# Optimization experiments

Measured on AMD Instinct MI355X. Metric: run time of the kernel, lower is better.

## Reference

```python
import jax, jax.numpy as jnp
import numpy as np

NH, HD, MB = 32, 64, 16        # heads, head_dim, TTT mini-batch size
BASE_LR = 1.0
ROPE_THETA = 10000.0


def _ln(x, w, b, eps):
    mu = x.mean(-1, keepdims=True)
    var = ((x - mu) ** 2).mean(-1, keepdims=True)
    return (x - mu) / jnp.sqrt(var + eps) * w + b


def _rotate_half(x):
    x1, x2 = jnp.split(x, 2, axis=-1)
    return jnp.concatenate([-x2, x1], axis=-1)


def _ln_l2_bwd(x, target, g, b, eps=1e-6):
    # grad of ||LN(x)*g+b - target||^2 / 2 wrt x (fused, as in ttt-lm)
    D = x.shape[-1]
    mu = x.mean(-1, keepdims=True)
    var = ((x - mu) ** 2).mean(-1, keepdims=True)
    std = jnp.sqrt(var + eps)
    xh = (x - mu) / std
    gxh = (g * xh + b - target) * g
    return (D * gxh - gxh.sum(-1, keepdims=True) - xh * (gxh * xh).sum(-1, keepdims=True)) / (D * std)


def _ttt_forward(x, q_w, k_w, v_w, o_w, ttt_lr_w, ttt_lr_b, token_idx_off,
                 ttt_norm_w, ttt_norm_b, W1, b1, post_w, post_b):
    B, L, C = x.shape
    NM = L // MB
    XQ = (x @ q_w).reshape(B, L, NH, HD).transpose(0, 2, 1, 3)  # [B,NH,L,HD]
    XK = (x @ k_w).reshape(B, L, NH, HD).transpose(0, 2, 1, 3)
    XV = (x @ v_w).reshape(B, L, NH, HD).transpose(0, 2, 1, 3)
    # rotary embedding at position_ids % mini_batch_size
    pos = (jnp.arange(L) % MB).astype(jnp.float32)
    inv = 1.0 / (ROPE_THETA ** (jnp.arange(0, HD, 2, dtype=jnp.float32) / HD))
    fr = pos[:, None] * inv[None, :]
    emb = jnp.concatenate([fr, fr], axis=-1)           # [L,HD]
    cos, sin = jnp.cos(emb), jnp.sin(emb)
    XQ = XQ * cos + _rotate_half(XQ) * sin
    XK = XK * cos + _rotate_half(XK) * sin
    # learning-rate gate (eta)
    Xm = x.reshape(B, NM, MB, C)
    ttt_lr = jax.nn.sigmoid(jnp.einsum('bnkc,hdc->bhnkd', Xm, ttt_lr_w)
                            + ttt_lr_b.reshape(1, NH, 1, 1, 1))       # [B,NH,NM,MB,1]
    ttt_lr_eta = BASE_LR * ttt_lr.transpose(0, 1, 2, 4, 3) / HD       # [B,NH,NM,1,MB]
    tok = jnp.maximum(1.0 / jnp.arange(1, MB + 1, dtype=jnp.float32) + token_idx_off, 0.0)
    eta = tok.reshape(1, 1, 1, MB, 1) * ttt_lr_eta                    # [B,NH,NM,MB,MB]

    def tomb(t):  # [B,NH,L,HD] -> [NM,B,NH,MB,HD]
        return t.reshape(B, NH, NM, MB, HD).transpose(2, 0, 1, 3, 4)

    xs = (tomb(XQ), tomb(XK), tomb(XV), eta.transpose(2, 0, 1, 3, 4))
    lw = ttt_norm_w.reshape(1, NH, 1, HD)
    lb = ttt_norm_b.reshape(1, NH, 1, HD)
    tril = jnp.tril(jnp.ones((MB, MB), x.dtype))
    W1s = jnp.broadcast_to(W1, (B, NH, HD, HD)).astype(x.dtype)
    b1s = jnp.broadcast_to(b1, (B, NH, 1, HD)).astype(x.dtype)

    def step(carry, xs_t):
        W1c, b1c = carry
        xq, xk, xv, et = xs_t                      # [B,NH,MB,HD], et [B,NH,MB,MB]
        Z1 = xk @ W1c + b1c
        grad = _ln_l2_bwd(Z1, xv - xk, lw, lb)     # grad of per-head TTT loss wrt Z1
        Attn1 = jnp.tril(xq @ xk.transpose(0, 1, 3, 2))
        b1_bar = b1c - (et * tril) @ grad
        Z1_bar = xq @ W1c - (et * Attn1) @ grad + b1_bar
        last_eta = et[:, :, -1, :, None]           # [B,NH,MB,1]
        W1n = W1c - jnp.einsum('bhki,bhkj->bhij', last_eta * xk, grad)
        b1n = b1c - (last_eta * grad).sum(-2, keepdims=True)
        out = xq + _ln(Z1_bar, lw, lb, 1e-6)
        return (W1n, b1n), out

    _, outs = jax.lax.scan(step, (W1s, b1s), xs)   # outs: [NM,B,NH,MB,HD]
    y = outs.transpose(1, 0, 3, 2, 4).reshape(B, L, C)
    y = _ln(y, post_w, post_b, 1e-6)
    return y @ o_w


def setup_inputs() -> dict:
    key = jax.random.key(0)
    ks = jax.random.split(key, 16)
    B, L, C, DH = 4, 2048, 2048, 1024
    s = 0.02
    return {
        'enc_input': jax.random.normal(ks[0], (B, L, C), jnp.float32),
        'ln1_w': jnp.ones((C,), jnp.float32), 'ln1_b': jnp.zeros((C,), jnp.float32),
        'q_w': jax.random.normal(ks[1], (C, C), jnp.float32) * s,
        'k_w': jax.random.normal(ks[2], (C, C), jnp.float32) * s,
        'v_w': jax.random.normal(ks[3], (C, C), jnp.float32) * s,
        'o_w': jax.random.normal(ks[4], (C, C), jnp.float32) * s,
        'ttt_lr_w': jax.random.normal(ks[5], (NH, 1, C), jnp.float32) * s,
        'ttt_lr_b': jax.random.normal(ks[6], (NH,), jnp.float32) * s,
        'token_idx_off': jax.random.normal(ks[7], (MB,), jnp.float32) * 0.01,
        'ttt_norm_w': jnp.ones((NH, HD), jnp.float32),
        'ttt_norm_b': jnp.zeros((NH, HD), jnp.float32),
        'W1': jax.random.normal(ks[8], (NH, HD, HD), jnp.float32) * s,
        'b1': jnp.zeros((NH, 1, HD), jnp.float32),
        'post_w': jnp.ones((C,), jnp.float32), 'post_b': jnp.zeros((C,), jnp.float32),
        'ffn_ln_w': jnp.ones((C,), jnp.float32), 'ffn_ln_b': jnp.zeros((C,), jnp.float32),
        'w1f': jax.random.normal(ks[9], (C, DH), jnp.float32) * s,
        'b1f': jnp.zeros((DH,), jnp.float32),
        'w2f': jax.random.normal(ks[10], (DH, C), jnp.float32) * s,
        'b2f': jnp.zeros((C,), jnp.float32),
    }


def reference(enc_input, ln1_w, ln1_b, q_w, k_w, v_w, o_w, ttt_lr_w, ttt_lr_b,
              token_idx_off, ttt_norm_w, ttt_norm_b, W1, b1, post_w, post_b,
              ffn_ln_w, ffn_ln_b, w1f, b1f, w2f, b2f):
    # pre-LN (torch default eps=1e-5) + TTT linear block + residual
    x = _ln(enc_input, ln1_w, ln1_b, 1e-5)
    y = _ttt_forward(x, q_w, k_w, v_w, o_w, ttt_lr_w, ttt_lr_b, token_idx_off,
                     ttt_norm_w, ttt_norm_b, W1, b1, post_w, post_b)
    y = y + enc_input
    # position-wise FFN (pre-LN eps=1e-6) + residual; dropout = eval no-op
    z = _ln(y, ffn_ln_w, ffn_ln_b, 1e-6)
    z = jax.nn.relu(z @ w1f + b1f) @ w2f + b2f
    return z + y
```

## Files before the change

kernel.cpp:

```cpp
#include <hip/hip_runtime.h>

typedef unsigned short u16;
typedef __attribute__((ext_vector_type(8))) short short8;
typedef __attribute__((ext_vector_type(8))) unsigned short ushort8;
typedef __attribute__((ext_vector_type(4))) float f32x4;
typedef __attribute__((ext_vector_type(2))) float f32x2;
typedef __attribute__((ext_vector_type(2))) unsigned int uint2v;

#define DEV __device__ __forceinline__

DEV float bf2f(u16 u){ union{unsigned int i; float f;} v; v.i = ((unsigned int)u)<<16u; return v.f; }
DEV u16 f2bf(float f){ union{float f; unsigned int i;} v; v.f=f; unsigned int r = v.i + 0x7FFFu + ((v.i>>16)&1u); return (u16)(r>>16); }

DEV void gload16(const u16* g, u16* l){
  __builtin_amdgcn_global_load_lds((const __attribute__((address_space(1))) void*)g,
                                   (__attribute__((address_space(3))) void*)l, 16, 0, 0);
}

DEV float wsum(float v){
  v += __shfl_xor(v, 32, 64);
  v += __shfl_xor(v, 16, 64);
  v += __shfl_xor(v, 8, 64);
  v += __shfl_xor(v, 4, 64);
  v += __shfl_xor(v, 2, 64);
  v += __shfl_xor(v, 1, 64);
  return v;
}

#if __has_builtin(__builtin_amdgcn_permlane16_swap) && __has_builtin(__builtin_amdgcn_permlane32_swap)
DEV float qsum(float v){
  unsigned u = __float_as_uint(v);
  uint2v a = __builtin_amdgcn_permlane16_swap(u, u, false, false);
  float s = __uint_as_float(a[0]) + __uint_as_float(a[1]);
  unsigned u2 = __float_as_uint(s);
  uint2v bsw = __builtin_amdgcn_permlane32_swap(u2, u2, false, false);
  return __uint_as_float(bsw[0]) + __uint_as_float(bsw[1]);
}
#else
DEV float qsum(float v){
  v += __shfl_xor(v, 16, 64);
  v += __shfl_xor(v, 32, 64);
  return v;
}
#endif

DEV float block_sum(float v, float* red){
  v = wsum(v);
  __syncthreads();
  if((threadIdx.x & 63u)==0) red[threadIdx.x>>6] = v;
  __syncthreads();
  return red[0]+red[1]+red[2]+red[3];
}

#define BARS() do{ asm volatile("s_waitcnt lgkmcnt(0)" ::: "memory"); \
  __builtin_amdgcn_s_barrier(); __builtin_amdgcn_sched_barrier(0); }while(0)

__global__ __launch_bounds__(256) void ln_row(
    const float* __restrict__ in, const float* __restrict__ w, const float* __restrict__ bb,
    float eps, u16* __restrict__ outb)
{
  __shared__ float red[4];
  const int row = blockIdx.x, t = threadIdx.x;
  const float* p = in + (size_t)row*2048 + t*8;
  f32x4 a = *(const f32x4*)p;
  f32x4 c = *(const f32x4*)(p+4);
  float s = a[0]+a[1]+a[2]+a[3]+c[0]+c[1]+c[2]+c[3];
  s = block_sum(s, red);
  float mu = s*(1.f/2048.f);
  float vs = 0.f;
  #pragma unroll
  for(int j=0;j<4;j++){ float d=a[j]-mu; vs += d*d; }
  #pragma unroll
  for(int j=0;j<4;j++){ float d=c[j]-mu; vs += d*d; }
  vs = block_sum(vs, red);
  float rstd = rsqrtf(vs*(1.f/2048.f) + eps);
  f32x4 w0 = *(const f32x4*)(w + t*8);
  f32x4 w1 = *(const f32x4*)(w + t*8 + 4);
  f32x4 b0 = *(const f32x4*)(bb + t*8);
  f32x4 b1 = *(const f32x4*)(bb + t*8 + 4);
  ushort8 o;
  #pragma unroll
  for(int j=0;j<4;j++) o[j]   = f2bf((a[j]-mu)*rstd*w0[j] + b0[j]);
  #pragma unroll
  for(int j=0;j<4;j++) o[j+4] = f2bf((c[j]-mu)*rstd*w1[j] + b1[j]);
  *(ushort8*)(outb + (size_t)row*2048 + t*8) = o;
}

__global__ __launch_bounds__(256) void transpose_cast(
    const float* __restrict__ src, u16* __restrict__ dst, int K, int N)
{
  __shared__ float tile[32][33];
  const int kb = blockIdx.x*32, nb = blockIdx.y*32;
  const int tx = threadIdx.x & 31, ty = threadIdx.x >> 5;
  #pragma unroll
  for(int i=0;i<4;i++){
    int k = ty + i*8;
    tile[k][tx] = src[(size_t)(kb+k)*N + nb + tx];
  }
  __syncthreads();
  #pragma unroll
  for(int i=0;i<4;i++){
    int nn = ty + i*8;
    dst[(size_t)(nb+nn)*K + kb + tx] = f2bf(tile[tx][nn]);
  }
}

__global__ __launch_bounds__(256) void cast_lrw(const float* __restrict__ lrw, u16* __restrict__ dst)
{
  int i = blockIdx.x*256 + threadIdx.x;
  if (i < 32*2048) dst[i] = f2bf(lrw[i]);
  else dst[i] = 0;
}

__global__ void rope_init(const float* __restrict__ tio, float* __restrict__ cosb,
                          float* __restrict__ sinb, float* __restrict__ tokb)
{
  int t = blockIdx.x*256 + threadIdx.x;
  if (t < 1024){
    int p = t>>6, d = t&63;
    float inv = powf(10000.f, -(float)(2*(d&31))/64.f);
    float fr = (float)p * inv;
    cosb[t] = cosf(fr);
    sinb[t] = sinf(fr);
  }
  if (blockIdx.x==0 && threadIdx.x<16)
    tokb[threadIdx.x] = fmaxf(1.f/(float)(threadIdx.x+1) + tio[threadIdx.x], 0.f);
}

#define MM(MI,NI,AA,BB) acc[MI][NI] = __builtin_amdgcn_mfma_f32_16x16x32_bf16(AA, BB, acc[MI][NI], 0, 0, 0)

#define RD_A(D,KH,MF) (*(const short8*)(ldsb + ((D)<<16) + ((KH)<<14) + (wm<<13) + ((MF)<<10) + loff))
#define RD_B(D,KH,NF) (*(const short8*)(ldsb + ((D)<<16) + 32768 + ((KH)<<14) + (wn<<12) + ((NF)<<10) + loff))

#define PHASE(D,KH,MH,RB,STG,VM) { \
  __builtin_amdgcn_sched_barrier(0); \
  if (RB){ b0 = RD_B(D,KH,0); b1 = RD_B(D,KH,1); b2 = RD_B(D,KH,2); b3 = RD_B(D,KH,3); } \
  short8 a0 = RD_A(D,KH,4*(MH)+0); \
  short8 a1 = RD_A(D,KH,4*(MH)+1); \
  short8 a2 = RD_A(D,KH,4*(MH)+2); \
  short8 a3 = RD_A(D,KH,4*(MH)+3); \
  STG; \
  __builtin_amdgcn_sched_barrier(0); \
  __builtin_amdgcn_s_barrier(); \
  asm volatile("s_waitcnt lgkmcnt(0)" ::: "memory"); \
  __builtin_amdgcn_sched_barrier(0); \
  __builtin_amdgcn_s_setprio(1); \
  MM(4*(MH)+0,0,a0,b0); MM(4*(MH)+1,0,a1,b0); MM(4*(MH)+2,0,a2,b0); MM(4*(MH)+3,0,a3,b0); \
  MM(4*(MH)+0,1,a0,b1); MM(4*(MH)+1,1,a1,b1); MM(4*(MH)+2,1,a2,b1); MM(4*(MH)+3,1,a3,b1); \
  MM(4*(MH)+0,2,a0,b2); MM(4*(MH)+1,2,a1,b2); MM(4*(MH)+2,2,a2,b2); MM(4*(MH)+3,2,a3,b2); \
  MM(4*(MH)+0,3,a0,b3); MM(4*(MH)+1,3,a1,b3); MM(4*(MH)+2,3,a2,b3); MM(4*(MH)+3,3,a3,b3); \
  __builtin_amdgcn_s_setprio(0); \
  if (VM){ asm volatile("s_waitcnt vmcnt(8)" ::: "memory"); } \
  __builtin_amdgcn_sched_barrier(0); \
  __builtin_amdgcn_s_barrier(); \
}

template<int EPI>
__global__ __launch_bounds__(512, 2) void gemm256(
    const u16* __restrict__ A, const u16* __restrict__ Bt,
    float* __restrict__ C, u16* __restrict__ Cb,
    const float* __restrict__ bias, const float* __restrict__ resid,
    int Nld, int Nreal, int K, int ntN)
{
  extern __shared__ u16 lds[];
  const int t = threadIdx.x, lane = t&63, wv = t>>6;
  const int wm = wv>>2, wn = wv&3;
  const int fr = lane&15, kq = lane>>4;

  int bid = blockIdx.x;
  {
    int nwg = gridDim.x;
    int q = nwg>>3, r = nwg&7;
    int x = bid&7, l = bid>>3;
    bid = (x<r) ? (x*(q+1)+l) : (r*(q+1)+(x-r)*q+l);
  }
  const int bm = bid/ntN, bn = bid%ntN;

  f32x4 acc[8][4];
  #pragma unroll
  for(int i=0;i<8;i++)
    #pragma unroll
    for(int j=0;j<4;j++) acc[i][j]=(f32x4){0.f,0.f,0.f,0.f};

  const u16* gA = A  + (size_t)(bm*256)*K;
  const u16* gB = Bt + (size_t)(bn*256)*K;

  const int Ls   = (t&7) ^ ((t>>3)&7);
  const int rstg = ((t>>3)<<1) | (Ls>>2);
  const int cstg = (Ls&3)<<3;
  u16* const ldsw = lds + (wv<<9);

  const int Plane = (((fr&1)<<2) | kq) ^ (fr>>1);
  const int loff  = ((fr>>1)<<7) | (Plane<<4);
  const char* const ldsb = (const char*)lds;

  auto stA = [&](int d, int kh, int kts){
    u16* lb = ldsw + (d<<15) + (kh<<13);
    const u16* g = gA + (size_t)rstg*K + kts + (kh<<5) + cstg;
    gload16(g, lb);
    gload16(g + ((size_t)K<<7), lb + 4096);
  };
  auto stB = [&](int d, int kh, int kts){
    u16* lb = ldsw + (d<<15) + 16384 + (kh<<13);
    const u16* g = gB + (size_t)rstg*K + kts + (kh<<5) + cstg;
    gload16(g, lb);
    gload16(g + ((size_t)K<<7), lb + 4096);
  };

  stA(0,0,0); stB(0,0,0); stA(0,1,0); stB(0,1,0); stA(1,0,64); stB(1,0,64);
  asm volatile("s_waitcnt vmcnt(8)" ::: "memory");
  __builtin_amdgcn_sched_barrier(0);
  __builtin_amdgcn_s_barrier();

  for (int kt = 0; kt < K; kt += 128){
    const int ktp = (kt+128 < K) ? kt+128 : 0;
    const int ktq = (kt+192 < K) ? kt+192 : kt+192-K;
    short8 b0={0},b1={0},b2={0},b3={0};
    PHASE(0,0,0,1, stA(1,1,kt+64), 0)
    PHASE(0,0,1,0, stB(1,1,kt+64), 1)
    PHASE(0,1,0,1, stA(0,0,ktp),   0)
    PHASE(0,1,1,0, stB(0,0,ktp),   1)
    PHASE(1,0,0,1, stA(0,1,ktp),   0)
    PHASE(1,0,1,0, stB(0,1,ktp),   1)
    PHASE(1,1,0,1, stA(1,0,ktq),   0)
    PHASE(1,1,1,0, stB(1,0,ktq),   1)
  }

  const int cr = (lane>>4)<<2, cc = lane&15;
  #pragma unroll
  for(int mi=0;mi<8;mi++){
    #pragma unroll
    for(int ni=0;ni<4;ni++){
      const int row0 = bm*256 + wm*128 + mi*16 + cr;
      const int col  = bn*256 + wn*64  + ni*16 + cc;
      if (col < Nreal){
        #pragma unroll
        for(int rr=0;rr<4;rr++){
          size_t idx = (size_t)(row0+rr)*Nld + col;
          float v = acc[mi][ni][rr];
          if (EPI==1 || EPI==3) v += resid[idx];
          if (EPI==2 || EPI==3) v += bias[col];
          if (EPI==2){ v = fmaxf(v, 0.f); Cb[idx] = f2bf(v); }
          else if (EPI==4){ Cb[idx] = f2bf(v); }
          else C[idx] = v;
        }
      }
    }
  }
}

#define W1LD 72
#define XLD  72
#define GTLD 40
#define EKLD 40
#define EALD 40
#define TLD  17

__global__ __launch_bounds__(512, 1) void ttt_scan(
    const u16* __restrict__ XQKV,
    const float* __restrict__ ropec, const float* __restrict__ ropes,
    const float* __restrict__ tokp,
    const float* __restrict__ nw, const float* __restrict__ nb,
    const float* __restrict__ lrb,
    const float* __restrict__ W1i,
    const float* __restrict__ b1i,
    float* __restrict__ Y)
{
  const int blk = blockIdx.x, b = blk>>5, h = blk&31;
  const int t = threadIdx.x, lane = t&63, wv = t>>6;
  const int fr = lane&15, quad = lane>>4;
  const int i0 = wv*2, i1 = i0+1;

  __shared__ u16 W1bf[2][64*W1LD];
  __shared__ u16 xqbf[2][16*XLD];
  __shared__ u16 xkbf[2][16*XLD];
  __shared__ u16 exkT[2][64*EKLD];
  __shared__ u16 gradTbf[64*GTLD];
  __shared__ u16 etaA[16*EALD];
  __shared__ float tgT[2][64*TLD];
  __shared__ float xqT[2][64*TLD];
  __shared__ float b1s[64];
  __shared__ f32x2 lwlb[64];
  __shared__ float lrs[2][16];
  __shared__ float tokl[16];

  const float lrbh = lrb[h];
  const float cc0 = ropec[i0*64 + lane], ss0 = ropes[i0*64 + lane];
  const float cc1 = ropec[i1*64 + lane], ss1 = ropes[i1*64 + lane];
  const float tok15 = tokp[15];
  const float ct = tok15*(1.f/64.f);
  const float sg = (lane<32)? -1.f : 1.f;

  f32x4 wf0, wf1, wf2, wf3;
  if (wv < 4){
    const float* wsrc = W1i + (size_t)h*4096;
    #pragma unroll
    for(int r=0;r<4;r++){
      int d = wv*16+quad*4+r;
      wf0[r] = wsrc[( 0+fr)*64 + d];
      wf1[r] = wsrc[(16+fr)*64 + d];
      wf2[r] = wsrc[(32+fr)*64 + d];
      wf3[r] = wsrc[(48+fr)*64 + d];
    }
    #pragma unroll
    for(int r=0;r<4;r++){
      int d = wv*16+quad*4+r;
      W1bf[0][d*W1LD +  0 + fr] = f2bf(wf0[r]);
      W1bf[0][d*W1LD + 16 + fr] = f2bf(wf1[r]);
      W1bf[0][d*W1LD + 32 + fr] = f2bf(wf2[r]);
      W1bf[0][d*W1LD + 48 + fr] = f2bf(wf3[r]);
    }
  }
  for(int i=t;i<64*24;i+=512){
    int rr=i/24, cp=16+i%24;
    gradTbf[rr*GTLD+cp]=0; exkT[0][rr*EKLD+cp]=0; exkT[1][rr*EKLD+cp]=0;
  }
  for(int i=t;i<16*24;i+=512){ int rr=i/24, cp=16+i%24; etaA[rr*EALD+cp]=0; }
  if (t<64){ b1s[t]=b1i[h*64+t]; lwlb[t]=(f32x2){nw[h*64+t], nb[h*64+t]}; }
  if (t<16) tokl[t]=tokp[t];

  auto stage = [&](int bf, u16 Pq0,u16 Pk0,u16 Pv0,u16 Pl0,
                           u16 Pq1,u16 Pk1,u16 Pv1,u16 Pl1){
    float q0=bf2f(Pq0), k0=bf2f(Pk0), v0=bf2f(Pv0);
    float q1=bf2f(Pq1), k1=bf2f(Pk1), v1=bf2f(Pv1);
    float qr0 = q0*cc0 + sg*__shfl_xor(q0,32,64)*ss0;
    float kr0 = k0*cc0 + sg*__shfl_xor(k0,32,64)*ss0;
    float qr1 = q1*cc1 + sg*__shfl_xor(q1,32,64)*ss1;
    float kr1 = k1*cc1 + sg*__shfl_xor(k1,32,64)*ss1;
    float lr0 = 1.f/(1.f + expf(-(bf2f(Pl0) + lrbh)));
    float lr1 = 1.f/(1.f + expf(-(bf2f(Pl1) + lrbh)));
    xqbf[bf][i0*XLD+lane] = f2bf(qr0);
    xqbf[bf][i1*XLD+lane] = f2bf(qr1);
    xkbf[bf][i0*XLD+lane] = f2bf(kr0);
    xkbf[bf][i1*XLD+lane] = f2bf(kr1);
    exkT[bf][lane*EKLD+i0] = f2bf(-ct*lr0*kr0);
    exkT[bf][lane*EKLD+i1] = f2bf(-ct*lr1*kr1);
    tgT[bf][lane*TLD+i0] = v0 - kr0;
    tgT[bf][lane*TLD+i1] = v1 - kr1;
    xqT[bf][lane*TLD+i0] = qr0;
    xqT[bf][lane*TLD+i1] = qr1;
    if (lane==0){ lrs[bf][i0]=lr0; lrs[bf][i1]=lr1; }
  };

  {
    const size_t rb = (size_t)b*2048;
    const u16* p0 = XQKV + (rb+i0)*6272 + h*64 + lane;
    const u16* p1 = XQKV + (rb+i1)*6272 + h*64 + lane;
    u16 l0 = XQKV[(rb+i0)*6272 + 6144 + h];
    u16 l1 = XQKV[(rb+i1)*6272 + 6144 + h];
    stage(0, p0[0],p0[2048],p0[4096],l0, p1[0],p1[2048],p1[4096],l1);
  }
  __syncthreads();

  const f32x4 fzero = (f32x4){0.f,0.f,0.f,0.f};

  for(int n=0;n<128;n++){
    const int cur = n&1, nxt = cur^1;
    const int cb = n&1, nbuf = cb^1;
    const size_t rbase = (size_t)b*2048 + n*16;

    u16 Pq0=0,Pk0=0,Pv0=0,Pl0=0,Pq1=0,Pk1=0,Pv1=0,Pl1=0;
    if (n<127){
      const size_t rb2 = rbase + 16;
      const u16* p0 = XQKV + (rb2+i0)*6272 + h*64 + lane;
      const u16* p1 = XQKV + (rb2+i1)*6272 + h*64 + lane;
      Pq0=p0[0]; Pk0=p0[2048]; Pv0=p0[4096];
      Pq1=p1[0]; Pk1=p1[2048]; Pv1=p1[4096];
      Pl0=XQKV[(rb2+i0)*6272 + 6144 + h];
      Pl1=XQKV[(rb2+i1)*6272 + 6144 + h];
    }

    f32x4 zq0, zq1, zq2, zq3;
    f32x4 b1q0, b1q1, b1q2, b1q3;
    float xq_r[16];
    f32x2 lw4[16];
    zq0=zq1=zq2=zq3=fzero; b1q0=b1q1=b1q2=b1q3=fzero;

    if (wv < 4){
      f32x4 b1v0 = *(const f32x4*)&b1s[ 0+quad*4];
      f32x4 b1v1 = *(const f32x4*)&b1s[16+quad*4];
      f32x4 b1v2 = *(const f32x4*)&b1s[32+quad*4];
      f32x4 b1v3 = *(const f32x4*)&b1s[48+quad*4];
      float tg[16]; f32x2 lwv[16];
      #pragma unroll
      for(int m=0;m<4;m++)
        #pragma unroll
        for(int r=0;r<4;r++){
          int d = m*16+quad*4+r;
          tg[m*4+r]  = tgT[cur][d*TLD + fr];
          lwv[m*4+r] = lwlb[d];
        }
      short8 bk0 = *(const short8*)&xkbf[cur][fr*XLD + quad*8];
      short8 bk1 = *(const short8*)&xkbf[cur][fr*XLD + 32 + quad*8];
      f32x4 z0,z1,z2,z3;
      z0 = __builtin_amdgcn_mfma_f32_16x16x32_bf16(*(const short8*)&W1bf[cb][( 0+fr)*W1LD + quad*8],      bk0, fzero, 0,0,0);
      z0 = __builtin_amdgcn_mfma_f32_16x16x32_bf16(*(const short8*)&W1bf[cb][( 0+fr)*W1LD + 32 + quad*8], bk1, z0,    0,0,0);
      z1 = __builtin_amdgcn_mfma_f32_16x16x32_bf16(*(const short8*)&W1bf[cb][(16+fr)*W1LD + quad*8],      bk0, fzero, 0,0,0);
      z1 = __builtin_amdgcn_mfma_f32_16x16x32_bf16(*(const short8*)&W1bf[cb][(16+fr)*W1LD + 32 + quad*8], bk1, z1,    0,0,0);
      z2 = __builtin_amdgcn_mfma_f32_16x16x32_bf16(*(const short8*)&W1bf[cb][(32+fr)*W1LD + quad*8],      bk0, fzero, 0,0,0);
      z2 = __builtin_amdgcn_mfma_f32_16x16x32_bf16(*(const short8*)&W1bf[cb][(32+fr)*W1LD + 32 + quad*8], bk1, z2,    0,0,0);
      z3 = __builtin_amdgcn_mfma_f32_16x16x32_bf16(*(const short8*)&W1bf[cb][(48+fr)*W1LD + quad*8],      bk0, fzero, 0,0,0);
      z3 = __builtin_amdgcn_mfma_f32_16x16x32_bf16(*(const short8*)&W1bf[cb][(48+fr)*W1LD + 32 + quad*8], bk1, z3,    0,0,0);
      f32x4 xh0,xh1,xh2,xh3;
      {
        float s1=0.f, s2=0.f;
        #pragma unroll
        for(int r=0;r<4;r++){
          z0[r] += b1v0[r];
          z1[r] += b1v1[r];
          z2[r] += b1v2[r];
          z3[r] += b1v3[r];
          s1 += z0[r]+z1[r]+z2[r]+z3[r];
          s2 += z0[r]*z0[r]+z1[r]*z1[r]+z2[r]*z2[r]+z3[r]*z3[r];
        }
        s1 = qsum(s1); s2 = qsum(s2);
        float mu = s1*(1.f/64.f);
        float var = s2*(1.f/64.f) - mu*mu;
        float rstd = rsqrtf(var + 1e-6f);
        float u1=0.f, u2=0.f;
        #pragma unroll
        for(int m=0;m<4;m++){
          f32x4* zp = (m==0)?&z0:(m==1)?&z1:(m==2)?&z2:&z3;
          f32x4* xp = (m==0)?&xh0:(m==1)?&xh1:(m==2)?&xh2:&xh3;
          #pragma unroll
          for(int r=0;r<4;r++){
            f32x2 wb = lwv[m*4+r];
            float xh = ((*zp)[r] - mu)*rstd;
            float gx = (wb[0]*xh + wb[1] - tg[m*4+r])*wb[0];
            (*xp)[r] = xh;
            (*zp)[r] = gx;
            u1 += gx; u2 += gx*xh;
          }
        }
        u1 = qsum(u1); u2 = qsum(u2);
        const float c64 = rstd*(1.f/64.f);
        #pragma unroll
        for(int m=0;m<4;m++){
          f32x4* zp = (m==0)?&z0:(m==1)?&z1:(m==2)?&z2:&z3;
          f32x4* xp = (m==0)?&xh0:(m==1)?&xh1:(m==2)?&xh2:&xh3;
          #pragma unroll
          for(int r=0;r<4;r++)
            (*zp)[r] = (64.f*(*zp)[r] - u1 - (*xp)[r]*u2)*c64;
        }
      }
      f32x4 zsel = (wv==0)?z0:(wv==1)?z1:(wv==2)?z2:z3;
      #pragma unroll
      for(int r=0;r<4;r++)
        gradTbf[(wv*16+quad*4+r)*GTLD + fr] = f2bf(zsel[r]);
      asm volatile("s_waitcnt lgkmcnt(0)" ::: "memory");
      short8 ga = *(const short8*)&gradTbf[(wv*16+fr)*GTLD + quad*8];
      short8 e0 = *(const short8*)&exkT[cur][( 0+fr)*EKLD + quad*8];
      short8 e1 = *(const short8*)&exkT[cur][(16+fr)*EKLD + quad*8];
      short8 e2 = *(const short8*)&exkT[cur][(32+fr)*EKLD + quad*8];
      short8 e3 = *(const short8*)&exkT[cur][(48+fr)*EKLD + quad*8];
      wf0 = __builtin_amdgcn_mfma_f32_16x16x32_bf16(ga, e0, wf0, 0,0,0);
      wf1 = __builtin_amdgcn_mfma_f32_16x16x32_bf16(ga, e1, wf1, 0,0,0);
      wf2 = __builtin_amdgcn_mfma_f32_16x16x32_bf16(ga, e2, wf2, 0,0,0);
      wf3 = __builtin_amdgcn_mfma_f32_16x16x32_bf16(ga, e3, wf3, 0,0,0);
      #pragma unroll
      for(int r=0;r<4;r++){
        int d = wv*16+quad*4+r;
        W1bf[nbuf][d*W1LD +  0 + fr] = f2bf(wf0[r]);
        W1bf[nbuf][d*W1LD + 16 + fr] = f2bf(wf1[r]);
        W1bf[nbuf][d*W1LD + 32 + fr] = f2bf(wf2[r]);
        W1bf[nbuf][d*W1LD + 48 + fr] = f2bf(wf3[r]);
      }
    }
    else if (wv == 4){
      b1q0 = *(const f32x4*)&b1s[ 0+quad*4];
      b1q1 = *(const f32x4*)&b1s[16+quad*4];
      b1q2 = *(const f32x4*)&b1s[32+quad*4];
      b1q3 = *(const f32x4*)&b1s[48+quad*4];
      #pragma unroll
      for(int m=0;m<4;m++)
        #pragma unroll
        for(int r=0;r<4;r++){
          int d = m*16+quad*4+r;
          xq_r[m*4+r] = xqT[cur][d*TLD + fr];
          lw4[m*4+r]  = lwlb[d];
        }
      short8 bq0 = *(const short8*)&xqbf[cur][fr*XLD + quad*8];
      short8 bq1 = *(const short8*)&xqbf[cur][fr*XLD + 32 + quad*8];
      zq0 = __builtin_amdgcn_mfma_f32_16x16x32_bf16(*(const short8*)&W1bf[cb][( 0+fr)*W1LD + quad*8],      bq0, fzero, 0,0,0);
      zq0 = __builtin_amdgcn_mfma_f32_16x16x32_bf16(*(const short8*)&W1bf[cb][( 0+fr)*W1LD + 32 + quad*8], bq1, zq0,   0,0,0);
      zq1 = __builtin_amdgcn_mfma_f32_16x16x32_bf16(*(const short8*)&W1bf[cb][(16+fr)*W1LD + quad*8],      bq0, fzero, 0,0,0);
      zq1 = __builtin_amdgcn_mfma_f32_16x16x32_bf16(*(const short8*)&W1bf[cb][(16+fr)*W1LD + 32 + quad*8], bq1, zq1,   0,0,0);
      zq2 = __builtin_amdgcn_mfma_f32_16x16x32_bf16(*(const short8*)&W1bf[cb][(32+fr)*W1LD + quad*8],      bq0, fzero, 0,0,0);
      zq2 = __builtin_amdgcn_mfma_f32_16x16x32_bf16(*(const short8*)&W1bf[cb][(32+fr)*W1LD + 32 + quad*8], bq1, zq2,   0,0,0);
      zq3 = __builtin_amdgcn_mfma_f32_16x16x32_bf16(*(const short8*)&W1bf[cb][(48+fr)*W1LD + quad*8],      bq0, fzero, 0,0,0);
      zq3 = __builtin_amdgcn_mfma_f32_16x16x32_bf16(*(const short8*)&W1bf[cb][(48+fr)*W1LD + 32 + quad*8], bq1, zq3,   0,0,0);
    }
    else if (wv == 7){
      short8 aq0 = *(const short8*)&xqbf[cur][fr*XLD + quad*8];
      short8 aq1 = *(const short8*)&xqbf[cur][fr*XLD + 32 + quad*8];
      short8 bk0 = *(const short8*)&xkbf[cur][fr*XLD + quad*8];
      short8 bk1 = *(const short8*)&xkbf[cur][fr*XLD + 32 + quad*8];
      f32x4 at;
      at = __builtin_amdgcn_mfma_f32_16x16x32_bf16(aq0, bk0, fzero, 0,0,0);
      at = __builtin_amdgcn_mfma_f32_16x16x32_bf16(aq1, bk1, at,    0,0,0);
      float lrj = lrs[cur][fr]*(1.f/64.f);
      #pragma unroll
      for(int r=0;r<4;r++){
        int i = quad*4 + r;
        float val = (fr <= i) ? -tokl[i]*lrj*(1.f + at[r]) : 0.f;
        etaA[i*EALD + fr] = f2bf(val);
      }
    }
    BARS();

    if (wv == 4){
      short8 be = *(const short8*)&etaA[fr*EALD + quad*8];
      f32x4 c20,c21,c22,c23;
      c20 = __builtin_amdgcn_mfma_f32_16x16x32_bf16(*(const short8*)&gradTbf[( 0+fr)*GTLD + quad*8], be, fzero, 0,0,0);
      c21 = __builtin_amdgcn_mfma_f32_16x16x32_bf16(*(const short8*)&gradTbf[(16+fr)*GTLD + quad*8], be, fzero, 0,0,0);
      c22 = __builtin_amdgcn_mfma_f32_16x16x32_bf16(*(const short8*)&gradTbf[(32+fr)*GTLD + quad*8], be, fzero, 0,0,0);
      c23 = __builtin_amdgcn_mfma_f32_16x16x32_bf16(*(const short8*)&gradTbf[(48+fr)*GTLD + quad*8], be, fzero, 0,0,0);
      f32x4 zb0,zb1,zb2,zb3;
      float s1=0.f, s2=0.f;
      #pragma unroll
      for(int r=0;r<4;r++){
        zb0[r] = zq0[r] + b1q0[r] + c20[r];
        zb1[r] = zq1[r] + b1q1[r] + c21[r];
        zb2[r] = zq2[r] + b1q2[r] + c22[r];
        zb3[r] = zq3[r] + b1q3[r] + c23[r];
        s1 += zb0[r]+zb1[r]+zb2[r]+zb3[r];
        s2 += zb0[r]*zb0[r]+zb1[r]*zb1[r]+zb2[r]*zb2[r]+zb3[r]*zb3[r];
      }
      s1 = qsum(s1); s2 = qsum(s2);
      float mu = s1*(1.f/64.f);
      float var = s2*(1.f/64.f) - mu*mu;
      float rstd = rsqrtf(var + 1e-6f);
      #pragma unroll
      for(int m=0;m<4;m++){
        f32x4* zp = (m==0)?&zb0:(m==1)?&zb1:(m==2)?&zb2:&zb3;
        f32x4 o;
        #pragma unroll
        for(int r=0;r<4;r++){
          f32x2 wb = lw4[m*4+r];
          float xh = ((*zp)[r] - mu)*rstd;
          o[r] = xq_r[m*4+r] + xh*wb[0] + wb[1];
        }
        *(f32x4*)&Y[(rbase+fr)*2048 + h*64 + m*16 + quad*4] = o;
      }
    }
    else if (wv == 5){
      const int d = lane;
      short8 g0 = *(const short8*)&gradTbf[d*GTLD + 0];
      short8 g1 = *(const short8*)&gradTbf[d*GTLD + 8];
      float s = 0.f;
      #pragma unroll
      for(int j=0;j<8;j++) s += lrs[cur][j]   * bf2f((u16)g0[j]);
      #pragma unroll
      for(int j=0;j<8;j++) s += lrs[cur][8+j] * bf2f((u16)g1[j]);
      b1s[d] -= ct * s;
    }
    if (n<127) stage(nxt, Pq0,Pk0,Pv0,Pl0, Pq1,Pk1,Pv1,Pl1);
    BARS();
  }
}

extern "C" void kernel_launch(void* const* d_in, const int* in_sizes, int n_in,
                              void* d_out, int out_size, void* d_ws, size_t ws_size,
                              hipStream_t stream)
{
  const float* enc   = (const float*)d_in[0];
  const float* ln1w  = (const float*)d_in[1];
  const float* ln1b  = (const float*)d_in[2];
  const float* qw    = (const float*)d_in[3];
  const float* kw    = (const float*)d_in[4];
  const float* vw    = (const float*)d_in[5];
  const float* ow    = (const float*)d_in[6];
  const float* lrw   = (const float*)d_in[7];
  const float* lrb   = (const float*)d_in[8];
  const float* tio   = (const float*)d_in[9];
  const float* tnw   = (const float*)d_in[10];
  const float* tnb   = (const float*)d_in[11];
  const float* W1i   = (const float*)d_in[12];
  const float* b1i   = (const float*)d_in[13];
  const float* postw = (const float*)d_in[14];
  const float* postb = (const float*)d_in[15];
  const float* flnw  = (const float*)d_in[16];
  const float* flnb  = (const float*)d_in[17];
  const float* w1f   = (const float*)d_in[18];
  const float* b1f   = (const float*)d_in[19];
  const float* w2f   = (const float*)d_in[20];
  const float* b2f   = (const float*)d_in[21];
  float* out = (float*)d_out;

  char* ws = (char*)d_ws;
  size_t off = 0;
  auto alloc = [&](size_t bytes)->void*{ void* p = ws + off; off += (bytes + 255) & ~(size_t)255; return p; };
  u16*   regA  = (u16*)  alloc(8192ull*2048*2);
  u16*   wqkvT = (u16*)  alloc(6400ull*2048*2);
  u16*   XQKV  = (u16*)  alloc(8192ull*6272*2);
  float* yb    = (float*)alloc(8192ull*2048*4);
  float* ropec = (float*)alloc(1024*4);
  float* ropes = (float*)alloc(1024*4);
  float* tokb  = (float*)alloc(64*4);

  u16* oT   = wqkvT;
  u16* w1fT = wqkvT + 2048ull*2048;
  u16* w2fT = w1fT + 1024ull*2048;
  u16* hbf  = XQKV;
  float* y2 = yb;

  static bool s_attr = false;
  if (!s_attr){
    s_attr = true;
    (void)hipFuncSetAttribute(reinterpret_cast<const void*>(gemm256<4>), hipFuncAttributeMaxDynamicSharedMemorySize, 131072);
    (void)hipFuncSetAttribute(reinterpret_cast<const void*>(gemm256<1>), hipFuncAttributeMaxDynamicSharedMemorySize, 131072);
    (void)hipFuncSetAttribute(reinterpret_cast<const void*>(gemm256<2>), hipFuncAttributeMaxDynamicSharedMemorySize, 131072);
    (void)hipFuncSetAttribute(reinterpret_cast<const void*>(gemm256<3>), hipFuncAttributeMaxDynamicSharedMemorySize, 131072);
  }

  rope_init<<<4, 256, 0, stream>>>(tio, ropec, ropes, tokb);

  dim3 tg1(64, 64);
  transpose_cast<<<tg1, 256, 0, stream>>>(qw, wqkvT,               2048, 2048);
  transpose_cast<<<tg1, 256, 0, stream>>>(kw, wqkvT + 2048ull*2048, 2048, 2048);
  transpose_cast<<<tg1, 256, 0, stream>>>(vw, wqkvT + 4096ull*2048, 2048, 2048);
  cast_lrw<<<2048, 256, 0, stream>>>(lrw, wqkvT + 6144ull*2048);

  ln_row<<<8192, 256, 0, stream>>>(enc, ln1w, ln1b, 1e-5f, regA);

  gemm256<4><<<32*25, 512, 131072, stream>>>(regA, wqkvT, nullptr, XQKV,
                                             nullptr, nullptr, 6272, 6272, 2048, 25);

  transpose_cast<<<tg1, 256, 0, stream>>>(ow, oT, 2048, 2048);
  dim3 tg2(64, 32);
  transpose_cast<<<tg2, 256, 0, stream>>>(w1f, w1fT, 2048, 1024);
  dim3 tg3(32, 64);
  transpose_cast<<<tg3, 256, 0, stream>>>(w2f, w2fT, 1024, 2048);

  ttt_scan<<<128, 512, 0, stream>>>(XQKV, ropec, ropes, tokb, tnw, tnb, lrb, W1i, b1i, yb);

  ln_row<<<8192, 256, 0, stream>>>(yb, postw, postb, 1e-6f, regA);
  gemm256<1><<<32*8, 512, 131072, stream>>>(regA, oT, y2, nullptr,
                                            nullptr, enc, 2048, 2048, 2048, 8);

  ln_row<<<8192, 256, 0, stream>>>(y2, flnw, flnb, 1e-6f, regA);
  gemm256<2><<<32*4, 512, 131072, stream>>>(regA, w1fT, nullptr, hbf,
                                            b1f, nullptr, 1024, 1024, 2048, 4);
  gemm256<3><<<32*8, 512, 131072, stream>>>(hbf, w2fT, out, nullptr,
                                            b2f, y2, 2048, 2048, 1024, 8);
}
```

Baseline: 857.1 us.

## Defer TTT output step by one mini-batch and split gradient across two waves

Restructures the per-mini-batch schedule in the TTT scan kernel. The output projection and norm for mini-batch n is deferred into iteration n+1, using double-buffered gradTbf and etaA, so it overlaps with the next gradient computation. The gradient/LN-backward work is also cut from four waves to two, with each producing two row blocks. Target and query tiles move to a row-major layout read with vector loads, and norm weights and token scales are kept in registers. This shortens the serial critical path per iteration at the cost of more shared memory and registers, and puts more work on fewer waves.

```diff
diff --git a/kernel.cpp b/kernel.cpp
--- a/kernel.cpp
+++ b/kernel.cpp
@@ -43,6 +43,8 @@
   return v;
 }
 #endif
+
+DEV float swap32(float v){ return __shfl_xor(v, 32, 64); }
 
 DEV float block_sum(float v, float* red){
   v = wsum(v);
@@ -254,7 +256,7 @@
 #define GTLD 40
 #define EKLD 40
 #define EALD 40
-#define TLD  17
+#define TD2  68
 
 __global__ __launch_bounds__(512, 1) void ttt_scan(
     const u16* __restrict__ XQKV,
@@ -275,21 +277,30 @@
   __shared__ u16 xqbf[2][16*XLD];
   __shared__ u16 xkbf[2][16*XLD];
   __shared__ u16 exkT[2][64*EKLD];
-  __shared__ u16 gradTbf[64*GTLD];
-  __shared__ u16 etaA[16*EALD];
-  __shared__ float tgT[2][64*TLD];
-  __shared__ float xqT[2][64*TLD];
+  __shared__ u16 gradTbf[2][64*GTLD];
+  __shared__ u16 etaA[2][16*EALD];
+  __shared__ float tgT2[2][16*TD2];
+  __shared__ float xqT2[2][16*TD2];
   __shared__ float b1s[64];
-  __shared__ f32x2 lwlb[64];
   __shared__ float lrs[2][16];
-  __shared__ float tokl[16];
 
   const float lrbh = lrb[h];
   const float cc0 = ropec[i0*64 + lane], ss0 = ropes[i0*64 + lane];
   const float cc1 = ropec[i1*64 + lane], ss1 = ropes[i1*64 + lane];
-  const float tok15 = tokp[15];
-  const float ct = tok15*(1.f/64.f);
+  const float ct = tokp[15]*(1.f/64.f);
   const float sg = (lane<32)? -1.f : 1.f;
+
+  f32x2 lwr[16];
+  #pragma unroll
+  for(int m=0;m<4;m++)
+    #pragma unroll
+    for(int r=0;r<4;r++){
+      int d = m*16+quad*4+r;
+      lwr[m*4+r] = (f32x2){nw[h*64+d], nb[h*64+d]};
+    }
+  float tki[4];
+  #pragma unroll
+  for(int r=0;r<4;r++) tki[r] = tokp[quad*4+r];
 
   f32x4 wf0, wf1, wf2, wf3;
   if (wv < 4){
@@ -313,20 +324,23 @@
   }
   for(int i=t;i<64*24;i+=512){
     int rr=i/24, cp=16+i%24;
-    gradTbf[rr*GTLD+cp]=0; exkT[0][rr*EKLD+cp]=0; exkT[1][rr*EKLD+cp]=0;
-  }
-  for(int i=t;i<16*24;i+=512){ int rr=i/24, cp=16+i%24; etaA[rr*EALD+cp]=0; }
-  if (t<64){ b1s[t]=b1i[h*64+t]; lwlb[t]=(f32x2){nw[h*64+t], nb[h*64+t]}; }
-  if (t<16) tokl[t]=tokp[t];
+    gradTbf[0][rr*GTLD+cp]=0; gradTbf[1][rr*GTLD+cp]=0;
+    exkT[0][rr*EKLD+cp]=0;    exkT[1][rr*EKLD+cp]=0;
+  }
+  for(int i=t;i<16*24;i+=512){
+    int rr=i/24, cp=16+i%24;
+    etaA[0][rr*EALD+cp]=0; etaA[1][rr*EALD+cp]=0;
+  }
+  if (t<64) b1s[t]=b1i[h*64+t];
 
   auto stage = [&](int bf, u16 Pq0,u16 Pk0,u16 Pv0,u16 Pl0,
                            u16 Pq1,u16 Pk1,u16 Pv1,u16 Pl1){
     float q0=bf2f(Pq0), k0=bf2f(Pk0), v0=bf2f(Pv0);
     float q1=bf2f(Pq1), k1=bf2f(Pk1), v1=bf2f(Pv1);
-    float qr0 = q0*cc0 + sg*__shfl_xor(q0,32,64)*ss0;
-    float kr0 = k0*cc0 + sg*__shfl_xor(k0,32,64)*ss0;
-    float qr1 = q1*cc1 + sg*__shfl_xor(q1,32,64)*ss1;
-    float kr1 = k1*cc1 + sg*__shfl_xor(k1,32,64)*ss1;
+    float qr0 = q0*cc0 + sg*swap32(q0)*ss0;
+    float kr0 = k0*cc0 + sg*swap32(k0)*ss0;
+    float qr1 = q1*cc1 + sg*swap32(q1)*ss1;
+    float kr1 = k1*cc1 + sg*swap32(k1)*ss1;
     float lr0 = 1.f/(1.f + expf(-(bf2f(Pl0) + lrbh)));
     float lr1 = 1.f/(1.f + expf(-(bf2f(Pl1) + lrbh)));
     xqbf[bf][i0*XLD+lane] = f2bf(qr0);
@@ -335,10 +349,10 @@
     xkbf[bf][i1*XLD+lane] = f2bf(kr1);
     exkT[bf][lane*EKLD+i0] = f2bf(-ct*lr0*kr0);
     exkT[bf][lane*EKLD+i1] = f2bf(-ct*lr1*kr1);
-    tgT[bf][lane*TLD+i0] = v0 - kr0;
-    tgT[bf][lane*TLD+i1] = v1 - kr1;
-    xqT[bf][lane*TLD+i0] = qr0;
-    xqT[bf][lane*TLD+i1] = qr1;
+    tgT2[bf][i0*TD2+lane] = v0 - kr0;
+    tgT2[bf][i1*TD2+lane] = v1 - kr1;
+    xqT2[bf][i0*TD2+lane] = qr0;
+    xqT2[bf][i1*TD2+lane] = qr1;
     if (lane==0){ lrs[bf][i0]=lr0; lrs[bf][i1]=lr1; }
   };
 
@@ -354,9 +368,53 @@
 
   const f32x4 fzero = (f32x4){0.f,0.f,0.f,0.f};
 
+  f32x4 zqP0=fzero, zqP1=fzero, zqP2=fzero, zqP3=fzero;
+  f32x4 b1qP0=fzero, b1qP1=fzero, b1qP2=fzero, b1qP3=fzero;
+
+  auto do_out = [&](int pbuf, size_t rb){
+    short8 be = *(const short8*)&etaA[pbuf][fr*EALD + quad*8];
+    f32x4 c20,c21,c22,c23;
+    c20 = __builtin_amdgcn_mfma_f32_16x16x32_bf16(*(const short8*)&gradTbf[pbuf][( 0+fr)*GTLD + quad*8], be, fzero, 0,0,0);
+    c21 = __builtin_amdgcn_mfma_f32_16x16x32_bf16(*(const short8*)&gradTbf[pbuf][(16+fr)*GTLD + quad*8], be, fzero, 0,0,0);
+    c22 = __builtin_amdgcn_mfma_f32_16x16x32_bf16(*(const short8*)&gradTbf[pbuf][(32+fr)*GTLD + quad*8], be, fzero, 0,0,0);
+    c23 = __builtin_amdgcn_mfma_f32_16x16x32_bf16(*(const short8*)&gradTbf[pbuf][(48+fr)*GTLD + quad*8], be, fzero, 0,0,0);
+    f32x4 xqv0 = *(const f32x4*)&xqT2[pbuf][fr*TD2 +  0 + quad*4];
+    f32x4 xqv1 = *(const f32x4*)&xqT2[pbuf][fr*TD2 + 16 + quad*4];
+    f32x4 xqv2 = *(const f32x4*)&xqT2[pbuf][fr*TD2 + 32 + quad*4];
+    f32x4 xqv3 = *(const f32x4*)&xqT2[pbuf][fr*TD2 + 48 + quad*4];
+    f32x4 zb0,zb1,zb2,zb3;
+    float s1=0.f, s2=0.f;
+    #pragma unroll
+    for(int r=0;r<4;r++){
+      zb0[r] = zqP0[r] + b1qP0[r] + c20[r];
+      zb1[r] = zqP1[r] + b1qP1[r] + c21[r];
+      zb2[r] = zqP2[r] + b1qP2[r] + c22[r];
+      zb3[r] = zqP3[r] + b1qP3[r] + c23[r];
+      s1 += zb0[r]+zb1[r]+zb2[r]+zb3[r];
+      s2 += zb0[r]*zb0[r]+zb1[r]*zb1[r]+zb2[r]*zb2[r]+zb3[r]*zb3[r];
+    }
+    s1 = qsum(s1); s2 = qsum(s2);
+    float mu = s1*(1.f/64.f);
+    float var = s2*(1.f/64.f) - mu*mu;
+    float rstd = rsqrtf(var + 1e-6f);
+    #pragma unroll
+    for(int m=0;m<4;m++){
+      f32x4* zp = (m==0)?&zb0:(m==1)?&zb1:(m==2)?&zb2:&zb3;
+      const f32x4* xp = (m==0)?&xqv0:(m==1)?&xqv1:(m==2)?&xqv2:&xqv3;
+      f32x4 o;
+      #pragma unroll
+      for(int r=0;r<4;r++){
+        f32x2 wb = lwr[m*4+r];
+        float xh = ((*zp)[r] - mu)*rstd;
+        o[r] = (*xp)[r] + xh*wb[0] + wb[1];
+      }
+      *(f32x4*)&Y[(rb+fr)*2048 + h*64 + m*16 + quad*4] = o;
+    }
+  };
+
   for(int n=0;n<128;n++){
-    const int cur = n&1, nxt = cur^1;
-    const int cb = n&1, nbuf = cb^1;
+    const int cur = n&1, nxt = cur^1, pb = cur^1;
+    const int cb = cur, nbuf = cur^1;
     const size_t rbase = (size_t)b*2048 + n*16;
 
     u16 Pq0=0,Pk0=0,Pv0=0,Pl0=0,Pq1=0,Pk1=0,Pv1=0,Pl1=0;
@@ -370,26 +428,15 @@
       Pl1=XQKV[(rb2+i1)*6272 + 6144 + h];
     }
 
-    f32x4 zq0, zq1, zq2, zq3;
-    f32x4 b1q0, b1q1, b1q2, b1q3;
-    float xq_r[16];
-    f32x2 lw4[16];
-    zq0=zq1=zq2=zq3=fzero; b1q0=b1q1=b1q2=b1q3=fzero;
-
-    if (wv < 4){
+    if (wv < 2){
       f32x4 b1v0 = *(const f32x4*)&b1s[ 0+quad*4];
       f32x4 b1v1 = *(const f32x4*)&b1s[16+quad*4];
       f32x4 b1v2 = *(const f32x4*)&b1s[32+quad*4];
       f32x4 b1v3 = *(const f32x4*)&b1s[48+quad*4];
-      float tg[16]; f32x2 lwv[16];
-      #pragma unroll
-      for(int m=0;m<4;m++)
-        #pragma unroll
-        for(int r=0;r<4;r++){
-          int d = m*16+quad*4+r;
-          tg[m*4+r]  = tgT[cur][d*TLD + fr];
-          lwv[m*4+r] = lwlb[d];
-        }
+      f32x4 tgv0 = *(const f32x4*)&tgT2[cur][fr*TD2 +  0 + quad*4];
+      f32x4 tgv1 = *(const f32x4*)&tgT2[cur][fr*TD2 + 16 + quad*4];
+      f32x4 tgv2 = *(const f32x4*)&tgT2[cur][fr*TD2 + 32 + quad*4];
+      f32x4 tgv3 = *(const f32x4*)&tgT2[cur][fr*TD2 + 48 + quad*4];
       short8 bk0 = *(const short8*)&xkbf[cur][fr*XLD + quad*8];
       short8 bk1 = *(const short8*)&xkbf[cur][fr*XLD + 32 + quad*8];
       f32x4 z0,z1,z2,z3;
@@ -422,11 +469,12 @@
         for(int m=0;m<4;m++){
           f32x4* zp = (m==0)?&z0:(m==1)?&z1:(m==2)?&z2:&z3;
           f32x4* xp = (m==0)?&xh0:(m==1)?&xh1:(m==2)?&xh2:&xh3;
+          const f32x4* tp = (m==0)?&tgv0:(m==1)?&tgv1:(m==2)?&tgv2:&tgv3;
           #pragma unroll
           for(int r=0;r<4;r++){
-            f32x2 wb = lwv[m*4+r];
+            f32x2 wb = lwr[m*4+r];
             float xh = ((*zp)[r] - mu)*rstd;
-            float gx = (wb[0]*xh + wb[1] - tg[m*4+r])*wb[0];
+            float gx = (wb[0]*xh + wb[1] - (*tp)[r])*wb[0];
             (*xp)[r] = xh;
             (*zp)[r] = gx;
             u1 += gx; u2 += gx*xh;
@@ -443,12 +491,54 @@
             (*zp)[r] = (64.f*(*zp)[r] - u1 - (*xp)[r]*u2)*c64;
         }
       }
-      f32x4 zsel = (wv==0)?z0:(wv==1)?z1:(wv==2)?z2:z3;
+      f32x4 zA = (wv==0)? z0 : z2;
+      f32x4 zB = (wv==0)? z1 : z3;
+      const int rb0 = wv*32;
       #pragma unroll
-      for(int r=0;r<4;r++)
-        gradTbf[(wv*16+quad*4+r)*GTLD + fr] = f2bf(zsel[r]);
-      asm volatile("s_waitcnt lgkmcnt(0)" ::: "memory");
-      short8 ga = *(const short8*)&gradTbf[(wv*16+fr)*GTLD + quad*8];
+      for(int r=0;r<4;r++){
+        gradTbf[cur][(rb0+quad*4+r)*GTLD + fr]    = f2bf(zA[r]);
+        gradTbf[cur][(rb0+16+quad*4+r)*GTLD + fr] = f2bf(zB[r]);
+      }
+    }
+    else if (wv == 4){
+      short8 bq0 = *(const short8*)&xqbf[cur][fr*XLD + quad*8];
+      short8 bq1 = *(const short8*)&xqbf[cur][fr*XLD + 32 + quad*8];
+      f32x4 zqN0,zqN1,zqN2,zqN3;
+      zqN0 = __builtin_amdgcn_mfma_f32_16x16x32_bf16(*(const short8*)&W1bf[cb][( 0+fr)*W1LD + quad*8],      bq0, fzero, 0,0,0);
+      zqN0 = __builtin_amdgcn_mfma_f32_16x16x32_bf16(*(const short8*)&W1bf[cb][( 0+fr)*W1LD + 32 + quad*8], bq1, zqN0,  0,0,0);
+      zqN1 = __builtin_amdgcn_mfma_f32_16x16x32_bf16(*(const short8*)&W1bf[cb][(16+fr)*W1LD + quad*8],      bq0, fzero, 0,0,0);
+      zqN1 = __builtin_amdgcn_mfma_f32_16x16x32_bf16(*(const short8*)&W1bf[cb][(16+fr)*W1LD + 32 + quad*8], bq1, zqN1,  0,0,0);
+      zqN2 = __builtin_amdgcn_mfma_f32_16x16x32_bf16(*(const short8*)&W1bf[cb][(32+fr)*W1LD + quad*8],      bq0, fzero, 0,0,0);
+      zqN2 = __builtin_amdgcn_mfma_f32_16x16x32_bf16(*(const short8*)&W1bf[cb][(32+fr)*W1LD + 32 + quad*8], bq1, zqN2,  0,0,0);
+      zqN3 = __builtin_amdgcn_mfma_f32_16x16x32_bf16(*(const short8*)&W1bf[cb][(48+fr)*W1LD + quad*8],      bq0, fzero, 0,0,0);
+      zqN3 = __builtin_amdgcn_mfma_f32_16x16x32_bf16(*(const short8*)&W1bf[cb][(48+fr)*W1LD + 32 + quad*8], bq1, zqN3,  0,0,0);
+      if (n > 0) do_out(pb, rbase - 16);
+      zqP0=zqN0; zqP1=zqN1; zqP2=zqN2; zqP3=zqN3;
+      b1qP0 = *(const f32x4*)&b1s[ 0+quad*4];
+      b1qP1 = *(const f32x4*)&b1s[16+quad*4];
+      b1qP2 = *(const f32x4*)&b1s[32+quad*4];
+      b1qP3 = *(const f32x4*)&b1s[48+quad*4];
+    }
+    else if (wv == 7){
+      short8 aq0 = *(const short8*)&xqbf[cur][fr*XLD + quad*8];
+      short8 aq1 = *(const short8*)&xqbf[cur][fr*XLD + 32 + quad*8];
+      short8 bk0 = *(const short8*)&xkbf[cur][fr*XLD + quad*8];
+      short8 bk1 = *(const short8*)&xkbf[cur][fr*XLD + 32 + quad*8];
+      f32x4 at;
+      at = __builtin_amdgcn_mfma_f32_16x16x32_bf16(aq0, bk0, fzero, 0,0,0);
+      at = __builtin_amdgcn_mfma_f32_16x16x32_bf16(aq1, bk1, at,    0,0,0);
+      float lrj = lrs[cur][fr]*(1.f/64.f);
+      #pragma unroll
+      for(int r=0;r<4;r++){
+        int i = quad*4 + r;
+        float val = (fr <= i) ? -tki[r]*lrj*(1.f + at[r]) : 0.f;
+        etaA[cur][i*EALD + fr] = f2bf(val);
+      }
+    }
+    BARS();
+
+    if (wv < 4){
+      short8 ga = *(const short8*)&gradTbf[cur][(wv*16+fr)*GTLD + quad*8];
       short8 e0 = *(const short8*)&exkT[cur][( 0+fr)*EKLD + quad*8];
       short8 e1 = *(const short8*)&exkT[cur][(16+fr)*EKLD + quad*8];
       short8 e2 = *(const short8*)&exkT[cur][(32+fr)*EKLD + quad*8];
@@ -466,87 +556,10 @@
         W1bf[nbuf][d*W1LD + 48 + fr] = f2bf(wf3[r]);
       }
     }
-    else if (wv == 4){
-      b1q0 = *(const f32x4*)&b1s[ 0+quad*4];
-      b1q1 = *(const f32x4*)&b1s[16+quad*4];
-      b1q2 = *(const f32x4*)&b1s[32+quad*4];
-      b1q3 = *(const f32x4*)&b1s[48+quad*4];
-      #pragma unroll
-      for(int m=0;m<4;m++)
-        #pragma unroll
-        for(int r=0;r<4;r++){
-          int d = m*16+quad*4+r;
-          xq_r[m*4+r] = xqT[cur][d*TLD + fr];
-          lw4[m*4+r]  = lwlb[d];
-        }
-      short8 bq0 = *(const short8*)&xqbf[cur][fr*XLD + quad*8];
-      short8 bq1 = *(const short8*)&xqbf[cur][fr*XLD + 32 + quad*8];
-      zq0 = __builtin_amdgcn_mfma_f32_16x16x32_bf16(*(const short8*)&W1bf[cb][( 0+fr)*W1LD + quad*8],      bq0, fzero, 0,0,0);
-      zq0 = __builtin_amdgcn_mfma_f32_16x16x32_bf16(*(const short8*)&W1bf[cb][( 0+fr)*W1LD + 32 + quad*8], bq1, zq0,   0,0,0);
-      zq1 = __builtin_amdgcn_mfma_f32_16x16x32_bf16(*(const short8*)&W1bf[cb][(16+fr)*W1LD + quad*8],      bq0, fzero, 0,0,0);
-      zq1 = __builtin_amdgcn_mfma_f32_16x16x32_bf16(*(const short8*)&W1bf[cb][(16+fr)*W1LD + 32 + quad*8], bq1, zq1,   0,0,0);
-      zq2 = __builtin_amdgcn_mfma_f32_16x16x32_bf16(*(const short8*)&W1bf[cb][(32+fr)*W1LD + quad*8],      bq0, fzero, 0,0,0);
-      zq2 = __builtin_amdgcn_mfma_f32_16x16x32_bf16(*(const short8*)&W1bf[cb][(32+fr)*W1LD + 32 + quad*8], bq1, zq2,   0,0,0);
-      zq3 = __builtin_amdgcn_mfma_f32_16x16x32_bf16(*(const short8*)&W1bf[cb][(48+fr)*W1LD + quad*8],      bq0, fzero, 0,0,0);
-      zq3 = __builtin_amdgcn_mfma_f32_16x16x32_bf16(*(const short8*)&W1bf[cb][(48+fr)*W1LD + 32 + quad*8], bq1, zq3,   0,0,0);
-    }
-    else if (wv == 7){
-      short8 aq0 = *(const short8*)&xqbf[cur][fr*XLD + quad*8];
-      short8 aq1 = *(const short8*)&xqbf[cur][fr*XLD + 32 + quad*8];
-      short8 bk0 = *(const short8*)&xkbf[cur][fr*XLD + quad*8];
-      short8 bk1 = *(const short8*)&xkbf[cur][fr*XLD + 32 + quad*8];
-      f32x4 at;
-      at = __builtin_amdgcn_mfma_f32_16x16x32_bf16(aq0, bk0, fzero, 0,0,0);
-      at = __builtin_amdgcn_mfma_f32_16x16x32_bf16(aq1, bk1, at,    0,0,0);
-      float lrj = lrs[cur][fr]*(1.f/64.f);
-      #pragma unroll
-      for(int r=0;r<4;r++){
-        int i = quad*4 + r;
-        float val = (fr <= i) ? -tokl[i]*lrj*(1.f + at[r]) : 0.f;
-        etaA[i*EALD + fr] = f2bf(val);
-      }
-    }
-    BARS();
-
-    if (wv == 4){
-      short8 be = *(const short8*)&etaA[fr*EALD + quad*8];
-      f32x4 c20,c21,c22,c23;
-      c20 = __builtin_amdgcn_mfma_f32_16x16x32_bf16(*(const short8*)&gradTbf[( 0+fr)*GTLD + quad*8], be, fzero, 0,0,0);
-      c21 = __builtin_amdgcn_mfma_f32_16x16x32_bf16(*(const short8*)&gradTbf[(16+fr)*GTLD + quad*8], be, fzero, 0,0,0);
-      c22 = __builtin_amdgcn_mfma_f32_16x16x32_bf16(*(const short8*)&gradTbf[(32+fr)*GTLD + quad*8], be, fzero, 0,0,0);
-      c23 = __builtin_amdgcn_mfma_f32_16x16x32_bf16(*(const short8*)&gradTbf[(48+fr)*GTLD + quad*8], be, fzero, 0,0,0);
-      f32x4 zb0,zb1,zb2,zb3;
-      float s1=0.f, s2=0.f;
-      #pragma unroll
-      for(int r=0;r<4;r++){
-        zb0[r] = zq0[r] + b1q0[r] + c20[r];
-        zb1[r] = zq1[r] + b1q1[r] + c21[r];
-        zb2[r] = zq2[r] + b1q2[r] + c22[r];
-        zb3[r] = zq3[r] + b1q3[r] + c23[r];
-        s1 += zb0[r]+zb1[r]+zb2[r]+zb3[r];
-        s2 += zb0[r]*zb0[r]+zb1[r]*zb1[r]+zb2[r]*zb2[r]+zb3[r]*zb3[r];
-      }
-      s1 = qsum(s1); s2 = qsum(s2);
-      float mu = s1*(1.f/64.f);
-      float var = s2*(1.f/64.f) - mu*mu;
-      float rstd = rsqrtf(var + 1e-6f);
-      #pragma unroll
-      for(int m=0;m<4;m++){
-        f32x4* zp = (m==0)?&zb0:(m==1)?&zb1:(m==2)?&zb2:&zb3;
-        f32x4 o;
-        #pragma unroll
-        for(int r=0;r<4;r++){
-          f32x2 wb = lw4[m*4+r];
-          float xh = ((*zp)[r] - mu)*rstd;
-          o[r] = xq_r[m*4+r] + xh*wb[0] + wb[1];
-        }
-        *(f32x4*)&Y[(rbase+fr)*2048 + h*64 + m*16 + quad*4] = o;
-      }
-    }
     else if (wv == 5){
       const int d = lane;
-      short8 g0 = *(const short8*)&gradTbf[d*GTLD + 0];
-      short8 g1 = *(const short8*)&gradTbf[d*GTLD + 8];
+      short8 g0 = *(const short8*)&gradTbf[cur][d*GTLD + 0];
+      short8 g1 = *(const short8*)&gradTbf[cur][d*GTLD + 8];
       float s = 0.f;
       #pragma unroll
       for(int j=0;j<8;j++) s += lrs[cur][j]   * bf2f((u16)g0[j]);
@@ -557,6 +570,8 @@
     if (n<127) stage(nxt, Pq0,Pk0,Pv0,Pl0, Pq1,Pk1,Pv1,Pl1);
     BARS();
   }
+
+  if (wv == 4) do_out(1, (size_t)b*2048 + 127*16);
 }
 
 extern "C" void kernel_launch(void* const* d_in, const int* in_sizes, int n_in,
```

Result: faster. 800.7 us (-6.6%).
